# Performance work log

Measured on AMD Instinct MI355X. Metric: run time of the kernel, lower is better.

The kernel has to match this reference:

```python
import jax, jax.numpy as jnp
import numpy as np

B, T, D = 2, 2048, 2048
H, KV, HD, RD = 16, 4, 128, 64  # n_heads, n_kv_heads, head_dim, rope_head_dim
THETA = 10000.0


def setup_inputs() -> dict:
    key = jax.random.key(0)
    ks = jax.random.split(key, 5)
    x = jax.random.normal(ks[0], (B, T, D), dtype=jnp.float32)
    Wq = jax.random.normal(ks[1], (D, H * HD), dtype=jnp.float32) * 0.02
    Wk = jax.random.normal(ks[2], (D, KV * HD), dtype=jnp.float32) * 0.02
    Wv = jax.random.normal(ks[3], (D, KV * HD), dtype=jnp.float32) * 0.02
    Wo = jax.random.normal(ks[4], (H * HD, D), dtype=jnp.float32) * 0.02
    # RoPE frequencies for the first RD dims of each head
    inv_freq = 1.0 / (THETA ** (jnp.arange(0, RD, 2, dtype=jnp.float32) / RD))  # [RD/2]
    ang = jnp.arange(T, dtype=jnp.float32)[:, None] * inv_freq[None, :]         # [T, RD/2]
    return {"x": x, "freqs_cos": jnp.cos(ang), "freqs_sin": jnp.sin(ang),
            "Wq": Wq, "Wk": Wk, "Wv": Wv, "Wo": Wo}


def _apply_rope(t, cos, sin):
    # t: [B, h, T, HD]; rotate first RD dims treating consecutive pairs as complex
    rot = t[..., :RD].reshape(*t.shape[:-1], RD // 2, 2)
    e, o = rot[..., 0], rot[..., 1]
    c = cos[None, None]  # [1,1,T,RD/2]
    s = sin[None, None]
    re = e * c - o * s
    ro = e * s + o * c
    rot_out = jnp.stack([re, ro], axis=-1).reshape(*t.shape[:-1], RD)
    return jnp.concatenate([rot_out, t[..., RD:]], axis=-1)


def reference(x, freqs_cos, freqs_sin, Wq, Wk, Wv, Wo):
    q = (x @ Wq).reshape(B, T, H, HD).transpose(0, 2, 1, 3)   # [B,H,T,HD]
    k = (x @ Wk).reshape(B, T, KV, HD).transpose(0, 2, 1, 3)  # [B,KV,T,HD]
    v = (x @ Wv).reshape(B, T, KV, HD).transpose(0, 2, 1, 3)
    q = _apply_rope(q, freqs_cos, freqs_sin)
    k = _apply_rope(k, freqs_cos, freqs_sin)
    present_k, present_v = k, v
    rep = H // KV
    kr = jnp.repeat(k, rep, axis=1)  # GQA repeat_interleave -> [B,H,T,HD]
    vr = jnp.repeat(v, rep, axis=1)
    scores = jnp.einsum('bhqd,bhkd->bhqk', q, kr) / jnp.sqrt(jnp.asarray(HD, q.dtype))
    causal = jnp.tril(jnp.ones((T, T), dtype=bool))
    scores = jnp.where(causal[None, None], scores, jnp.asarray(-1e9, scores.dtype))
    attn = jax.nn.softmax(scores, axis=-1)
    y = jnp.einsum('bhqk,bhkd->bhqd', attn, vr)
    y = y.transpose(0, 2, 1, 3).reshape(B, T, H * HD) @ Wo  # [B,T,D]
    return y, present_k, present_v
```

## Files before the change

### kernel.cpp

```cpp
#include <hip/hip_runtime.h>
#include <hip/hip_bf16.h>

static constexpr int B_  = 2;
static constexpr int T_  = 2048;
static constexpr int D_  = 2048;
static constexpr int H_  = 16;
static constexpr int KV_ = 4;
static constexpr int HD_ = 128;
static constexpr int RD_ = 64;
static constexpr int BT_ = B_ * T_;
static constexpr int NPROJ_ = 3072;
static constexpr float SCALE_ = 0.08838834764831845f;

typedef __attribute__((ext_vector_type(8))) short bf16x8;
typedef __attribute__((ext_vector_type(8))) unsigned short u16x8;
typedef __attribute__((ext_vector_type(4))) float f32x4;

#define COMPILER_BARRIER() __asm__ __volatile__("" ::: "memory")
#define BAR() do { COMPILER_BARRIER(); __builtin_amdgcn_s_barrier(); COMPILER_BARRIER(); } while (0)

typedef const __attribute__((address_space(1))) unsigned int* as1_u32p;
typedef __attribute__((address_space(3))) unsigned int* as3_u32p;
#define GLOAD16(g, l) __builtin_amdgcn_global_load_lds((as1_u32p)(const void*)(g), (as3_u32p)(void*)(l), 16, 0, 0)

__device__ __forceinline__ unsigned short f2bu(float f) {
  unsigned x = __float_as_uint(f);
  unsigned r = (x + 0x7fffu + ((x >> 16) & 1u)) >> 16;
  return (unsigned short)r;
}

__global__ __launch_bounds__(256) void cvt_bf16(const float* __restrict__ in,
                                                unsigned short* __restrict__ out) {
  const size_t i = ((size_t)blockIdx.x * 256 + threadIdx.x) * 4;
  const float4 f = *(const float4*)(in + i);
  ushort4 o;
  o.x = f2bu(f.x); o.y = f2bu(f.y); o.z = f2bu(f.z); o.w = f2bu(f.w);
  *(ushort4*)(out + i) = o;
}

__global__ __launch_bounds__(256) void t32_all(const float* __restrict__ Wq,
                                               const float* __restrict__ Wk,
                                               const float* __restrict__ Wv,
                                               const float* __restrict__ Wo,
                                               unsigned short* __restrict__ Wqt,
                                               unsigned short* __restrict__ Wkvt,
                                               unsigned short* __restrict__ Wot) {
  const float* in; unsigned short* out; int C;
  switch (blockIdx.z) {
    case 0:  in = Wq; out = Wqt;                       C = 2048; break;
    case 1:  in = Wk; out = Wkvt;                      C = 512;  break;
    case 2:  in = Wv; out = Wkvt + (size_t)512 * D_;   C = 512;  break;
    default: in = Wo; out = Wot;                       C = 2048; break;
  }
  if ((int)blockIdx.y * 32 >= C) return;

  __shared__ unsigned short tile[32][36];
  const int r0 = blockIdx.x * 32;
  const int c0 = blockIdx.y * 32;
  const int tid = threadIdx.x;
  {
    const int r = tid >> 3;
    const int c = (tid & 7) * 4;
    const float4 f = *(const float4*)(in + (size_t)(r0 + r) * C + c0 + c);
    ushort4 w;
    w.x = f2bu(f.x); w.y = f2bu(f.y); w.z = f2bu(f.z); w.w = f2bu(f.w);
    *(ushort4*)&tile[r][c] = w;
  }
  __syncthreads();
  {
    const int c = tid >> 3;
    const int r = (tid & 7) * 4;
    ushort4 o;
    o.x = tile[r + 0][c];
    o.y = tile[r + 1][c];
    o.z = tile[r + 2][c];
    o.w = tile[r + 3][c];
    *(ushort4*)(out + (size_t)(c0 + c) * D_ + r0 + r) = o;
  }
}

template <int EPI>
__global__ __launch_bounds__(512, 1) void gemm256(const unsigned short* __restrict__ A,
                                                  const unsigned short* __restrict__ Bt,
                                                  float* __restrict__ C,
                                                  unsigned short* __restrict__ Qbf,
                                                  float* __restrict__ kout,
                                                  float* __restrict__ vout,
                                                  unsigned short* __restrict__ Kbf,
                                                  const float* __restrict__ cosb,
                                                  const float* __restrict__ sinb,
                                                  int N) {
  __shared__ __align__(16) unsigned short As[2][256 * 64];
  __shared__ __align__(16) unsigned short Bs[2][256 * 64];
  constexpr int K = D_;
  constexpr int KT = K / 64;

  const int tid = threadIdx.x;
  const int lane = tid & 63;
  const int wave = tid >> 6;
  const int n16 = lane & 15;
  const int quad = lane >> 4;
  const int wm = wave >> 2;
  const int wn = wave & 3;

  const int nwg = gridDim.x * gridDim.y;
  int bid = blockIdx.y * gridDim.x + blockIdx.x;
  bid = (bid & 7) * (nwg >> 3) + (bid >> 3);
  const int bn = (bid % (int)gridDim.x) * 256;
  const int bm = (bid / (int)gridDim.x) * 256;

  const int t8 = tid >> 3;
  const int kg = ((tid & 7) ^ (t8 & 7)) << 3;
  const unsigned short *aS0[2], *aS1[2], *bS0[2], *bS1[2];
#pragma unroll
  for (int g = 0; g < 2; ++g) {
    aS0[g] = A + (size_t)(bm + g * 128 + t8) * K + kg;
    aS1[g] = A + (size_t)(bm + g * 128 + 64 + t8) * K + kg;
    const int br = (g * 2 + (t8 >> 5)) * 64 + (t8 & 31);
    bS0[g] = Bt + (size_t)(bn + br) * K + kg;
    bS1[g] = Bt + (size_t)(bn + br + 32) * K + kg;
  }

#define STAGE(dst, half, src, koff)                                             \
  do {                                                                          \
    GLOAD16((src)[0] + (koff), &(dst)[((half) * 128 + 0) * 64 + wave * 512]);   \
    GLOAD16((src)[1] + (koff), &(dst)[((half) * 128 + 64) * 64 + wave * 512]);  \
  } while (0)

#define LDA_(DST, MH)                                                             \
  _Pragma("unroll") for (int ks = 0; ks < 2; ++ks)                                \
  _Pragma("unroll") for (int i = 0; i < 4; ++i)                                   \
      DST[ks][i] = *(const bf16x8*)&cA[((MH) * 128 + wm * 64 + i * 16 + n16) * 64 \
                                       + ((quad * 8 + ks * 32) ^ ((n16 & 7) << 3))];

#define LDB_(DST, NH)                                                             \
  _Pragma("unroll") for (int ks = 0; ks < 2; ++ks)                                \
  _Pragma("unroll") for (int jj = 0; jj < 2; ++jj)                                \
      DST[ks][jj] = *(const bf16x8*)&cB[((NH) * 128 + wn * 32 + jj * 16 + n16) * 64 \
                                        + ((quad * 8 + ks * 32) ^ ((n16 & 7) << 3))];

#define MFQ(MH, NH, AF, BF)                                                       \
  do {                                                                            \
    __builtin_amdgcn_s_setprio(1);                                                \
    _Pragma("unroll") for (int ks = 0; ks < 2; ++ks)                              \
    _Pragma("unroll") for (int i = 0; i < 4; ++i)                                 \
    _Pragma("unroll") for (int jj = 0; jj < 2; ++jj)                              \
        acc[(MH) * 4 + i][(NH) * 2 + jj] = __builtin_amdgcn_mfma_f32_16x16x32_bf16( \
            AF[ks][i], BF[ks][jj], acc[(MH) * 4 + i][(NH) * 2 + jj], 0, 0, 0);    \
    __builtin_amdgcn_s_setprio(0);                                                \
  } while (0)

  f32x4 acc[8][4];
#pragma unroll
  for (int mi = 0; mi < 8; ++mi)
#pragma unroll
    for (int ni = 0; ni < 4; ++ni) acc[mi][ni] = (f32x4){0.f, 0.f, 0.f, 0.f};

  bf16x8 aF[2][4], aG[2][4], b0F[2][2], b1F[2][2];

  STAGE(As[0], 0, aS0, 0);
  STAGE(Bs[0], 0, bS0, 0);
  STAGE(Bs[0], 1, bS1, 0);
  STAGE(As[0], 1, aS1, 0);

  for (int kt = 0; kt < KT - 1; ++kt) {
    const unsigned short* cA = As[kt & 1];
    const unsigned short* cB = Bs[kt & 1];
    unsigned short* nA = As[(kt & 1) ^ 1];
    unsigned short* nB = Bs[(kt & 1) ^ 1];
    const int ko = (kt + 1) * 64;

    STAGE(nA, 0, aS0, ko);
    STAGE(nB, 0, bS0, ko);
    STAGE(nB, 1, bS1, ko);
    STAGE(nA, 1, aS1, ko);
    asm volatile("s_waitcnt vmcnt(8)" ::: "memory");
    BAR();

    LDA_(aF, 0);
    LDB_(b0F, 0);
    LDB_(b1F, 1);
    MFQ(0, 0, aF, b0F);
    LDA_(aG, 1);
    MFQ(0, 1, aF, b1F);
    MFQ(1, 1, aG, b1F);
    MFQ(1, 0, aG, b0F);

    BAR();
  }

  {
    const unsigned short* cA = As[(KT - 1) & 1];
    const unsigned short* cB = Bs[(KT - 1) & 1];
    asm volatile("s_waitcnt vmcnt(0)" ::: "memory");
    BAR();
    LDA_(aF, 0);
    LDB_(b0F, 0);
    LDB_(b1F, 1);
    MFQ(0, 0, aF, b0F);
    LDA_(aG, 1);
    MFQ(0, 1, aF, b1F);
    MFQ(1, 1, aG, b1F);
    MFQ(1, 0, aG, b0F);
  }

#pragma unroll
  for (int mi = 0; mi < 8; ++mi) {
#pragma unroll
    for (int rr = 0; rr < 4; ++rr) {
      const int row = bm + wm * 128 + mi * 16 + quad * 4 + rr;
      if (EPI == 0) {
#pragma unroll
        for (int ni = 0; ni < 4; ++ni) {
          const int col = bn + wn * 64 + ni * 16 + n16;
          C[(size_t)row * N + col] = acc[mi][ni][rr];
        }
      } else {
        const int b = row >> 11, t = row & (T_ - 1);
#pragma unroll
        for (int ni = 0; ni < 4; ++ni) {
          const int col = bn + wn * 64 + ni * 16 + n16;
          const int hd = col & 127;
          float v = acc[mi][ni][rr];
          const float other = __shfl_xor(v, 1);
          if (col < 2560 && hd < RD_) {
            const float c = cosb[t * 32 + (hd >> 1)];
            const float s = sinb[t * 32 + (hd >> 1)];
            v = (col & 1) ? (other * s + v * c) : (v * c - other * s);
          }
          if (col < 2048) {
            Qbf[(size_t)row * (H_ * HD_) + col] = f2bu(v * SCALE_);
          } else if (col < 2560) {
            const int kv = (col - 2048) >> 7;
            const size_t idx = (((size_t)(b * KV_ + kv) * T_) + t) * HD_ + hd;
            kout[idx] = v;
            Kbf[idx] = f2bu(v);
          } else {
            const int kv = (col - 2560) >> 7;
            vout[(((size_t)(b * KV_ + kv) * T_) + t) * HD_ + hd] = v;
          }
        }
      }
    }
  }
#undef STAGE
#undef LDA_
#undef LDB_
#undef MFQ
}

__global__ __launch_bounds__(256) void v_transpose(const float* __restrict__ vin,
                                                   unsigned short* __restrict__ vt) {
  __shared__ unsigned int tile[32][17];
  const int tid = threadIdx.x;
  const int k0 = blockIdx.x * 32;
  const int d0 = blockIdx.y * 32;
  const int g  = blockIdx.z;
  const float* src = vin + ((size_t)g * T_ + k0) * HD_ + d0;

  {
    const int kr = tid >> 3;
    const int d2 = (tid & 7) * 2;
#pragma unroll
    for (int c = 0; c < 2; ++c) {
      const float2 f = *(const float2*)(src + (size_t)kr * HD_ + (d2 + c) * 2);
      tile[kr][d2 + c] = (unsigned)f2bu(f.x) | ((unsigned)f2bu(f.y) << 16);
    }
  }
  __syncthreads();
  {
    const int dr = tid >> 3;
    const int kc = (tid & 7) * 4;
    const int dstb = ((kc & 15) << 1) | ((kc & 16) >> 2);
    const int hi = dr >> 1;
    const int sh = (dr & 1) * 16;
    ushort4 o;
    o.x = (unsigned short)(tile[kc + 0][hi] >> sh);
    o.y = (unsigned short)(tile[kc + 1][hi] >> sh);
    o.z = (unsigned short)(tile[kc + 2][hi] >> sh);
    o.w = (unsigned short)(tile[kc + 3][hi] >> sh);
    *(ushort4*)(vt + ((size_t)g * HD_ + d0 + dr) * T_ + k0 + dstb) = o;
  }
}

__global__ __launch_bounds__(256, 2) void attn_flash(const unsigned short* __restrict__ Q,
                                                     const unsigned short* __restrict__ Kbf,
                                                     const unsigned short* __restrict__ VbfT,
                                                     unsigned short* __restrict__ O) {
  __shared__ __align__(16) unsigned short Ks[32 * 128];
  __shared__ __align__(16) unsigned short Vs[128 * 32];

  const int tid = threadIdx.x;
  const int wave = tid >> 6;
  const int lane = tid & 63;
  const int n16 = lane & 15;
  const int quad = lane >> 4;
  const int pid = blockIdx.x;
  const int q0A = pid * 16;
  const int q0B = (127 - pid) * 16;
  const int nchA = (q0A + 47) >> 5;
  const int nchB = (q0B + 47) >> 5;
  const int bkv = blockIdx.y;
  const int b = bkv >> 2;
  const int kvh = bkv & 3;
  const int h = kvh * 4 + wave;

  const unsigned short* ksrc = Kbf + ((size_t)(b * KV_ + kvh)) * T_ * HD_;
  const unsigned short* vtsrc = VbfT + ((size_t)(b * KV_ + kvh)) * HD_ * T_;

  const int krow = tid >> 4;
  const int kcol = (tid & 15) * 8;
  const int kdst0 = (krow * 128 + kcol) ^ ((krow & 7) << 3);
  const int kdst1 = ((krow + 16) * 128 + kcol) ^ ((krow & 7) << 3);
  const int vrow = tid >> 2;
  const int vcol = (tid & 3) * 8;
  const int vdst0 = (vrow * 32 + vcol) ^ ((vrow & 3) << 3);
  const int vdst1 = ((vrow + 64) * 32 + vcol) ^ ((vrow & 3) << 3);

  bf16x8 qfA[4], qfB[4];
  {
    const unsigned short* qa = Q + ((size_t)(b * T_ + q0A + n16)) * (H_ * HD_) + h * HD_ + quad * 8;
    const unsigned short* qb = Q + ((size_t)(b * T_ + q0B + n16)) * (H_ * HD_) + h * HD_ + quad * 8;
#pragma unroll
    for (int s = 0; s < 4; ++s) {
      qfA[s] = *(const bf16x8*)(qa + s * 32);
      qfB[s] = *(const bf16x8*)(qb + s * 32);
    }
  }

  float mA = -1e30f, lA = 0.f;
  float mB = -1e30f, lB = 0.f;
  f32x4 oA[8], oB[8];
#pragma unroll
  for (int t = 0; t < 8; ++t) { oA[t] = (f32x4){0.f,0.f,0.f,0.f}; oB[t] = (f32x4){0.f,0.f,0.f,0.f}; }

  {
    const u16x8 ka = *(const u16x8*)(ksrc + (size_t)krow * HD_ + kcol);
    const u16x8 kb = *(const u16x8*)(ksrc + (size_t)(krow + 16) * HD_ + kcol);
    const u16x8 va = *(const u16x8*)(vtsrc + (size_t)vrow * T_ + vcol);
    const u16x8 vb = *(const u16x8*)(vtsrc + (size_t)(vrow + 64) * T_ + vcol);
    *(u16x8*)&Ks[kdst0] = ka;
    *(u16x8*)&Ks[kdst1] = kb;
    *(u16x8*)&Vs[vdst0] = va;
    *(u16x8*)&Vs[vdst1] = vb;
  }
  __syncthreads();

  for (int c = 0; c < nchB; ++c) {
    const int kc = c * 32;
    const bool actA = (c < nchA);

    u16x8 ka, kb, va, vb;
    if (c + 1 < nchB) {
      ka = *(const u16x8*)(ksrc + (size_t)(kc + 32 + krow) * HD_ + kcol);
      kb = *(const u16x8*)(ksrc + (size_t)(kc + 48 + krow) * HD_ + kcol);
      va = *(const u16x8*)(vtsrc + (size_t)vrow * T_ + (kc + 32) + vcol);
      vb = *(const u16x8*)(vtsrc + (size_t)(vrow + 64) * T_ + (kc + 32) + vcol);
    }
    COMPILER_BARRIER();

    f32x4 sB0 = (f32x4){0.f,0.f,0.f,0.f}, sB1 = sB0, sA0 = sB0, sA1 = sB0;
#pragma unroll
    for (int s = 0; s < 4; ++s) {
      const bf16x8 kf0 = *(const bf16x8*)&Ks[(n16 * 128 + quad * 8 + s * 32) ^ ((n16 & 7) << 3)];
      const bf16x8 kf1 = *(const bf16x8*)&Ks[((16 + n16) * 128 + quad * 8 + s * 32) ^ ((n16 & 7) << 3)];
      sB0 = __builtin_amdgcn_mfma_f32_16x16x32_bf16(kf0, qfB[s], sB0, 0, 0, 0);
      sB1 = __builtin_amdgcn_mfma_f32_16x16x32_bf16(kf1, qfB[s], sB1, 0, 0, 0);
      if (actA) {
        sA0 = __builtin_amdgcn_mfma_f32_16x16x32_bf16(kf0, qfA[s], sA0, 0, 0, 0);
        sA1 = __builtin_amdgcn_mfma_f32_16x16x32_bf16(kf1, qfA[s], sA1, 0, 0, 0);
      }
    }

    union { bf16x8 v; unsigned short u[8]; } pkB, pkA;
    bool growB;
    float alphaB = 1.f, alphaA = 1.f;
    {
      float s[8];
#pragma unroll
      for (int r = 0; r < 4; ++r) { s[r] = sB0[r]; s[r + 4] = sB1[r]; }
      if (c == nchB - 1) {
        const int qrow = q0B + n16;
#pragma unroll
        for (int r = 0; r < 4; ++r) {
          if (kc + quad * 4 + r > qrow)      s[r]     = -1e30f;
          if (kc + 16 + quad * 4 + r > qrow) s[r + 4] = -1e30f;
        }
      }
      float mm = fmaxf(fmaxf(fmaxf(s[0], s[1]), fmaxf(s[2], s[3])),
                       fmaxf(fmaxf(s[4], s[5]), fmaxf(s[6], s[7])));
      mm = fmaxf(mm, __shfl_xor(mm, 16));
      mm = fmaxf(mm, __shfl_xor(mm, 32));
      growB = __any(mm > mB);
      if (growB) {
        const float mnew = fmaxf(mB, mm);
        alphaB = __expf(mB - mnew);
        mB = mnew;
      }
      float lsum = 0.f;
#pragma unroll
      for (int j = 0; j < 8; ++j) {
        const float p = __expf(s[j] - mB);
        lsum += p;
        pkB.u[j] = f2bu(p);
      }
      lsum += __shfl_xor(lsum, 16);
      lsum += __shfl_xor(lsum, 32);
      lB = growB ? (alphaB * lB + lsum) : (lB + lsum);
    }

    bool growA = false;
    if (actA) {
      float s[8];
#pragma unroll
      for (int r = 0; r < 4; ++r) { s[r] = sA0[r]; s[r + 4] = sA1[r]; }
      if (c == nchA - 1) {
        const int qrow = q0A + n16;
#pragma unroll
        for (int r = 0; r < 4; ++r) {
          if (kc + quad * 4 + r > qrow)      s[r]     = -1e30f;
          if (kc + 16 + quad * 4 + r > qrow) s[r + 4] = -1e30f;
        }
      }
      float mm = fmaxf(fmaxf(fmaxf(s[0], s[1]), fmaxf(s[2], s[3])),
                       fmaxf(fmaxf(s[4], s[5]), fmaxf(s[6], s[7])));
      mm = fmaxf(mm, __shfl_xor(mm, 16));
      mm = fmaxf(mm, __shfl_xor(mm, 32));
      growA = __any(mm > mA);
      if (growA) {
        const float mnew = fmaxf(mA, mm);
        alphaA = __expf(mA - mnew);
        mA = mnew;
      }
      float lsum = 0.f;
#pragma unroll
      for (int j = 0; j < 8; ++j) {
        const float p = __expf(s[j] - mA);
        lsum += p;
        pkA.u[j] = f2bu(p);
      }
      lsum += __shfl_xor(lsum, 16);
      lsum += __shfl_xor(lsum, 32);
      lA = growA ? (alphaA * lA + lsum) : (lA + lsum);
    }

    if (growB) {
      f32x4 av;
#pragma unroll
      for (int r = 0; r < 4; ++r) av[r] = __shfl(alphaB, quad * 4 + r);
#pragma unroll
      for (int t = 0; t < 8; ++t) {
        oB[t][0] *= av[0]; oB[t][1] *= av[1]; oB[t][2] *= av[2]; oB[t][3] *= av[3];
      }
    }
    if (growA) {
      f32x4 av;
#pragma unroll
      for (int r = 0; r < 4; ++r) av[r] = __shfl(alphaA, quad * 4 + r);
#pragma unroll
      for (int t = 0; t < 8; ++t) {
        oA[t][0] *= av[0]; oA[t][1] *= av[1]; oA[t][2] *= av[2]; oA[t][3] *= av[3];
      }
    }

#pragma unroll
    for (int t = 0; t < 8; ++t) {
      const bf16x8 vf = *(const bf16x8*)&Vs[((t * 16 + n16) * 32 + quad * 8) ^ ((n16 & 3) << 3)];
      oB[t] = __builtin_amdgcn_mfma_f32_16x16x32_bf16(pkB.v, vf, oB[t], 0, 0, 0);
      if (actA) oA[t] = __builtin_amdgcn_mfma_f32_16x16x32_bf16(pkA.v, vf, oA[t], 0, 0, 0);
    }

    __syncthreads();
    if (c + 1 < nchB) {
      *(u16x8*)&Ks[kdst0] = ka;
      *(u16x8*)&Ks[kdst1] = kb;
      *(u16x8*)&Vs[vdst0] = va;
      *(u16x8*)&Vs[vdst1] = vb;
    }
    __syncthreads();
  }

  {
    unsigned short* obB = O + ((size_t)(b * T_ + q0B)) * (H_ * HD_) + h * HD_;
    unsigned short* obA = O + ((size_t)(b * T_ + q0A)) * (H_ * HD_) + h * HD_;
#pragma unroll
    for (int r = 0; r < 4; ++r) {
      const float liB = 1.0f / __shfl(lB, quad * 4 + r);
      const float liA = 1.0f / __shfl(lA, quad * 4 + r);
#pragma unroll
      for (int t = 0; t < 8; ++t) {
        obB[(size_t)(quad * 4 + r) * (H_ * HD_) + t * 16 + n16] = f2bu(oB[t][r] * liB);
        obA[(size_t)(quad * 4 + r) * (H_ * HD_) + t * 16 + n16] = f2bu(oA[t][r] * liA);
      }
    }
  }
}

extern "C" void kernel_launch(void* const* d_in, const int* in_sizes, int n_in,
                              void* d_out, int out_size, void* d_ws, size_t ws_size,
                              hipStream_t stream) {
  const float* x  = (const float*)d_in[0];
  const float* fc = (const float*)d_in[1];
  const float* fs = (const float*)d_in[2];
  const float* Wq = (const float*)d_in[3];
  const float* Wk = (const float*)d_in[4];
  const float* Wv = (const float*)d_in[5];
  const float* Wo = (const float*)d_in[6];

  float* yout = (float*)d_out;
  float* kout = yout + (size_t)B_ * T_ * D_;
  float* vout = kout + (size_t)B_ * KV_ * T_ * HD_;
  unsigned short* Qbf = (unsigned short*)yout;

  unsigned short* xb   = (unsigned short*)d_ws;
  unsigned short* Abf  = xb;
  unsigned short* Wqt  = xb   + (size_t)BT_ * D_;
  unsigned short* Wkvt = Wqt  + (size_t)D_ * D_;
  unsigned short* Wot  = Wkvt + (size_t)1024 * D_;
  unsigned short* Kbf  = Wot  + (size_t)D_ * D_;
  unsigned short* VbfT = Kbf  + (size_t)B_ * KV_ * T_ * HD_;

  dim3 blk(256);

  cvt_bf16<<<dim3((BT_ * D_) / 1024), blk, 0, stream>>>(x, xb);
  t32_all<<<dim3(D_ / 32, D_ / 32, 4), blk, 0, stream>>>(Wq, Wk, Wv, Wo, Wqt, Wkvt, Wot);

  gemm256<1><<<dim3(NPROJ_ / 256, BT_ / 256), dim3(512), 0, stream>>>(
      xb, Wqt, nullptr, Qbf, kout, vout, Kbf, fc, fs, NPROJ_);

  v_transpose<<<dim3(T_ / 32, HD_ / 32, B_ * KV_), blk, 0, stream>>>(vout, VbfT);

  attn_flash<<<dim3(64, B_ * KV_), blk, 0, stream>>>(Qbf, Kbf, VbfT, Abf);

  gemm256<0><<<dim3(D_ / 256, BT_ / 256), dim3(512), 0, stream>>>(
      Abf, Wot, yout, nullptr, nullptr, nullptr, nullptr, nullptr, nullptr, D_);
}
```

Before: 386.2 us.

## Shrink GEMM tiles to 128x128 with 256 threads and two blocks per CU

Replaces the 256x256, 512-thread GEMM with a 128x128 tile kernel run by 4 waves, each computing a 64x64 sub-tile. Shared memory is halved and launch bounds allow two blocks per CU. The grid becomes four times larger, which fills the 256 CUs better: the old grid had only 192 and 128 blocks for the two GEMMs. The trade-off is lower arithmetic intensity per tile and more global/L2 traffic for operands.

```diff
diff --git a/kernel.cpp b/kernel.cpp
--- a/kernel.cpp
+++ b/kernel.cpp
@@ -80,7 +80,7 @@
 }
 
 template <int EPI>
-__global__ __launch_bounds__(512, 1) void gemm256(const unsigned short* __restrict__ A,
+__global__ __launch_bounds__(256, 2) void gemm128(const unsigned short* __restrict__ A,
                                                   const unsigned short* __restrict__ Bt,
                                                   float* __restrict__ C,
                                                   unsigned short* __restrict__ Qbf,
@@ -90,8 +90,8 @@
                                                   const float* __restrict__ cosb,
                                                   const float* __restrict__ sinb,
                                                   int N) {
-  __shared__ __align__(16) unsigned short As[2][256 * 64];
-  __shared__ __align__(16) unsigned short Bs[2][256 * 64];
+  __shared__ __align__(16) unsigned short As[2][128 * 64];
+  __shared__ __align__(16) unsigned short Bs[2][128 * 64];
   constexpr int K = D_;
   constexpr int KT = K / 64;
 
@@ -100,68 +100,65 @@
   const int wave = tid >> 6;
   const int n16 = lane & 15;
   const int quad = lane >> 4;
-  const int wm = wave >> 2;
-  const int wn = wave & 3;
+  const int wm = wave >> 1;
+  const int wn = wave & 1;
 
   const int nwg = gridDim.x * gridDim.y;
   int bid = blockIdx.y * gridDim.x + blockIdx.x;
   bid = (bid & 7) * (nwg >> 3) + (bid >> 3);
-  const int bn = (bid % (int)gridDim.x) * 256;
-  const int bm = (bid / (int)gridDim.x) * 256;
-
-  const int t8 = tid >> 3;
-  const int kg = ((tid & 7) ^ (t8 & 7)) << 3;
-  const unsigned short *aS0[2], *aS1[2], *bS0[2], *bS1[2];
-#pragma unroll
-  for (int g = 0; g < 2; ++g) {
-    aS0[g] = A + (size_t)(bm + g * 128 + t8) * K + kg;
-    aS1[g] = A + (size_t)(bm + g * 128 + 64 + t8) * K + kg;
-    const int br = (g * 2 + (t8 >> 5)) * 64 + (t8 & 31);
-    bS0[g] = Bt + (size_t)(bn + br) * K + kg;
-    bS1[g] = Bt + (size_t)(bn + br + 32) * K + kg;
-  }
-
-#define STAGE(dst, half, src, koff)                                             \
-  do {                                                                          \
-    GLOAD16((src)[0] + (koff), &(dst)[((half) * 128 + 0) * 64 + wave * 512]);   \
-    GLOAD16((src)[1] + (koff), &(dst)[((half) * 128 + 64) * 64 + wave * 512]);  \
+  const int bn = (bid % (int)gridDim.x) * 128;
+  const int bm = (bid / (int)gridDim.x) * 128;
+
+  const int t5 = tid >> 3;
+  const int kg = ((tid & 7) ^ (t5 & 7)) << 3;
+  const unsigned short *aS[4], *bS[4];
+#pragma unroll
+  for (int g = 0; g < 4; ++g) {
+    aS[g] = A  + (size_t)(bm + g * 32 + t5) * K + kg;
+    bS[g] = Bt + (size_t)(bn + g * 32 + t5) * K + kg;
+  }
+
+#define STAGE_A(dst, koff)                                     \
+  _Pragma("unroll") for (int g = 0; g < 4; ++g)                \
+      GLOAD16(aS[g] + (koff), &(dst)[g * 2048 + wave * 512]);
+
+#define STAGE_B(dst, koff)                                     \
+  _Pragma("unroll") for (int g = 0; g < 4; ++g)                \
+      GLOAD16(bS[g] + (koff), &(dst)[g * 2048 + wave * 512]);
+
+#define LDFRAGS(cA, cB)                                                             \
+  do {                                                                              \
+    _Pragma("unroll") for (int ks = 0; ks < 2; ++ks)                                \
+    _Pragma("unroll") for (int i = 0; i < 4; ++i)                                   \
+        aF[ks][i] = *(const bf16x8*)&(cA)[(wm * 64 + i * 16 + n16) * 64             \
+                                          + ((quad * 8 + ks * 32) ^ ((n16 & 7) << 3))]; \
+    _Pragma("unroll") for (int ks = 0; ks < 2; ++ks)                                \
+    _Pragma("unroll") for (int jj = 0; jj < 4; ++jj)                                \
+        bF[ks][jj] = *(const bf16x8*)&(cB)[(wn * 64 + jj * 16 + n16) * 64           \
+                                           + ((quad * 8 + ks * 32) ^ ((n16 & 7) << 3))]; \
   } while (0)
 
-#define LDA_(DST, MH)                                                             \
-  _Pragma("unroll") for (int ks = 0; ks < 2; ++ks)                                \
-  _Pragma("unroll") for (int i = 0; i < 4; ++i)                                   \
-      DST[ks][i] = *(const bf16x8*)&cA[((MH) * 128 + wm * 64 + i * 16 + n16) * 64 \
-                                       + ((quad * 8 + ks * 32) ^ ((n16 & 7) << 3))];
-
-#define LDB_(DST, NH)                                                             \
-  _Pragma("unroll") for (int ks = 0; ks < 2; ++ks)                                \
-  _Pragma("unroll") for (int jj = 0; jj < 2; ++jj)                                \
-      DST[ks][jj] = *(const bf16x8*)&cB[((NH) * 128 + wn * 32 + jj * 16 + n16) * 64 \
-                                        + ((quad * 8 + ks * 32) ^ ((n16 & 7) << 3))];
-
-#define MFQ(MH, NH, AF, BF)                                                       \
-  do {                                                                            \
-    __builtin_amdgcn_s_setprio(1);                                                \
-    _Pragma("unroll") for (int ks = 0; ks < 2; ++ks)                              \
-    _Pragma("unroll") for (int i = 0; i < 4; ++i)                                 \
-    _Pragma("unroll") for (int jj = 0; jj < 2; ++jj)                              \
-        acc[(MH) * 4 + i][(NH) * 2 + jj] = __builtin_amdgcn_mfma_f32_16x16x32_bf16( \
-            AF[ks][i], BF[ks][jj], acc[(MH) * 4 + i][(NH) * 2 + jj], 0, 0, 0);    \
-    __builtin_amdgcn_s_setprio(0);                                                \
+#define MFALL()                                                                     \
+  do {                                                                              \
+    __builtin_amdgcn_s_setprio(1);                                                  \
+    _Pragma("unroll") for (int ks = 0; ks < 2; ++ks)                                \
+    _Pragma("unroll") for (int i = 0; i < 4; ++i)                                   \
+    _Pragma("unroll") for (int jj = 0; jj < 4; ++jj)                                \
+        acc[i][jj] = __builtin_amdgcn_mfma_f32_16x16x32_bf16(                       \
+            aF[ks][i], bF[ks][jj], acc[i][jj], 0, 0, 0);                            \
+    __builtin_amdgcn_s_setprio(0);                                                  \
   } while (0)
 
-  f32x4 acc[8][4];
-#pragma unroll
-  for (int mi = 0; mi < 8; ++mi)
+  f32x4 acc[4][4];
+#pragma unroll
+  for (int mi = 0; mi < 4; ++mi)
 #pragma unroll
     for (int ni = 0; ni < 4; ++ni) acc[mi][ni] = (f32x4){0.f, 0.f, 0.f, 0.f};
 
-  bf16x8 aF[2][4], aG[2][4], b0F[2][2], b1F[2][2];
-
-  STAGE(As[0], 0, aS0, 0);
-  STAGE(Bs[0], 0, bS0, 0);
-  STAGE(Bs[0], 1, bS1, 0);
-  STAGE(As[0], 1, aS1, 0);
+  bf16x8 aF[2][4], bF[2][4];
+
+  STAGE_A(As[0], 0);
+  STAGE_B(Bs[0], 0);
 
   for (int kt = 0; kt < KT - 1; ++kt) {
     const unsigned short* cA = As[kt & 1];
@@ -170,21 +167,13 @@
     unsigned short* nB = Bs[(kt & 1) ^ 1];
     const int ko = (kt + 1) * 64;
 
-    STAGE(nA, 0, aS0, ko);
-    STAGE(nB, 0, bS0, ko);
-    STAGE(nB, 1, bS1, ko);
-    STAGE(nA, 1, aS1, ko);
+    STAGE_A(nA, ko);
+    STAGE_B(nB, ko);
     asm volatile("s_waitcnt vmcnt(8)" ::: "memory");
     BAR();
 
-    LDA_(aF, 0);
-    LDB_(b0F, 0);
-    LDB_(b1F, 1);
-    MFQ(0, 0, aF, b0F);
-    LDA_(aG, 1);
-    MFQ(0, 1, aF, b1F);
-    MFQ(1, 1, aG, b1F);
-    MFQ(1, 0, aG, b0F);
+    LDFRAGS(cA, cB);
+    MFALL();
 
     BAR();
   }
@@ -194,21 +183,15 @@
     const unsigned short* cB = Bs[(KT - 1) & 1];
     asm volatile("s_waitcnt vmcnt(0)" ::: "memory");
     BAR();
-    LDA_(aF, 0);
-    LDB_(b0F, 0);
-    LDB_(b1F, 1);
-    MFQ(0, 0, aF, b0F);
-    LDA_(aG, 1);
-    MFQ(0, 1, aF, b1F);
-    MFQ(1, 1, aG, b1F);
-    MFQ(1, 0, aG, b0F);
-  }
-
-#pragma unroll
-  for (int mi = 0; mi < 8; ++mi) {
+    LDFRAGS(cA, cB);
+    MFALL();
+  }
+
+#pragma unroll
+  for (int mi = 0; mi < 4; ++mi) {
 #pragma unroll
     for (int rr = 0; rr < 4; ++rr) {
-      const int row = bm + wm * 128 + mi * 16 + quad * 4 + rr;
+      const int row = bm + wm * 64 + mi * 16 + quad * 4 + rr;
       if (EPI == 0) {
 #pragma unroll
         for (int ni = 0; ni < 4; ++ni) {
@@ -243,10 +226,10 @@
       }
     }
   }
-#undef STAGE
-#undef LDA_
-#undef LDB_
-#undef MFQ
+#undef STAGE_A
+#undef STAGE_B
+#undef LDFRAGS
+#undef MFALL
 }
 
 __global__ __launch_bounds__(256) void v_transpose(const float* __restrict__ vin,
@@ -525,13 +508,13 @@
   cvt_bf16<<<dim3((BT_ * D_) / 1024), blk, 0, stream>>>(x, xb);
   t32_all<<<dim3(D_ / 32, D_ / 32, 4), blk, 0, stream>>>(Wq, Wk, Wv, Wo, Wqt, Wkvt, Wot);
 
-  gemm256<1><<<dim3(NPROJ_ / 256, BT_ / 256), dim3(512), 0, stream>>>(
+  gemm128<1><<<dim3(NPROJ_ / 128, BT_ / 128), blk, 0, stream>>>(
       xb, Wqt, nullptr, Qbf, kout, vout, Kbf, fc, fs, NPROJ_);
 
   v_transpose<<<dim3(T_ / 32, HD_ / 32, B_ * KV_), blk, 0, stream>>>(vout, VbfT);
 
   attn_flash<<<dim3(64, B_ * KV_), blk, 0, stream>>>(Qbf, Kbf, VbfT, Abf);
 
-  gemm256<0><<<dim3(D_ / 256, BT_ / 256), dim3(512), 0, stream>>>(
+  gemm128<0><<<dim3(D_ / 128, BT_ / 128), blk, 0, stream>>>(
       Abf, Wot, yout, nullptr, nullptr, nullptr, nullptr, nullptr, nullptr, D_);
 }
```

Result: faster. 364.6 us (-5.6%).
